# Kernel tuning notes

Measured on AMD Instinct MI355X. Metric: run time of the kernel, lower is better.

The kernel has to match this reference:

```python
import jax, jax.numpy as jnp
import numpy as np

B, S, D, H = 2, 2048, 2048, 16
DK = D // H  # 128
ROPE_BASE = 10000.0


def _rope_tables(seq_len, d_k, dtype=jnp.float32):
    # cos/sin of shape [1, S, 1, d_k], duplicated halves as in the torch module
    inv_freq = 1.0 / (ROPE_BASE ** (jnp.arange(0, d_k, 2, dtype=jnp.float32) / d_k))
    pos = jnp.arange(seq_len, dtype=jnp.float32)
    freqs = jnp.outer(pos, inv_freq)               # [S, d_k/2]
    cos = jnp.concatenate([jnp.cos(freqs), jnp.cos(freqs)], axis=-1)  # [S, d_k]
    sin = jnp.concatenate([jnp.sin(freqs), jnp.sin(freqs)], axis=-1)
    return cos[None, :, None, :].astype(dtype), sin[None, :, None, :].astype(dtype)


def _rotate_half(x):
    d = x.shape[-1]
    x1, x2 = x[..., : d // 2], x[..., d // 2 :]
    return jnp.concatenate([-x2, x1], axis=-1)


def setup_inputs() -> dict:
    key = jax.random.key(0)
    ks = jax.random.split(key, 5)
    scale = 1.0 / np.sqrt(D)
    x = jax.random.normal(ks[0], (B, S, D), dtype=jnp.float32)
    Wq = jax.random.normal(ks[1], (D, D), dtype=jnp.float32) * scale
    Wk = jax.random.normal(ks[2], (D, D), dtype=jnp.float32) * scale
    Wv = jax.random.normal(ks[3], (D, D), dtype=jnp.float32) * scale
    Wo = jax.random.normal(ks[4], (D, D), dtype=jnp.float32) * scale
    bq = jnp.zeros((D,), jnp.float32)
    bk = jnp.zeros((D,), jnp.float32)
    bv = jnp.zeros((D,), jnp.float32)
    bo = jnp.zeros((D,), jnp.float32)
    mask = jnp.tril(jnp.ones((S, S), dtype=bool))[None, None]  # causal [1,1,S,S]
    return {"x": x, "mask": mask, "Wq": Wq, "bq": bq, "Wk": Wk, "bk": bk,
            "Wv": Wv, "bv": bv, "Wo": Wo, "bo": bo}


def reference(x, mask, Wq, bq, Wk, bk, Wv, bv, Wo, bo):
    b, s, d = x.shape
    # torch nn.Linear: y = x @ W.T + b
    Q = (x @ Wq.T + bq).reshape(b, s, H, DK)
    K = (x @ Wk.T + bk).reshape(b, s, H, DK)
    V = (x @ Wv.T + bv).reshape(b, s, H, DK)
    cos, sin = _rope_tables(s, DK, x.dtype)
    Q = Q * cos + _rotate_half(Q) * sin
    K = K * cos + _rotate_half(K) * sin
    # [b, h, s, dk]
    Q = Q.transpose(0, 2, 1, 3)
    K = K.transpose(0, 2, 1, 3)
    V = V.transpose(0, 2, 1, 3)
    scores = jnp.einsum("bhqd,bhkd->bhqk", Q, K) / jnp.sqrt(jnp.asarray(DK, x.dtype))
    scores = jnp.where(mask, scores, jnp.asarray(-jnp.inf, x.dtype))
    attn = jax.nn.softmax(scores, axis=-1)
    out = jnp.einsum("bhqk,bhkd->bhqd", attn, V)
    out = out.transpose(0, 2, 1, 3).reshape(b, s, d)
    return out @ Wo.T + bo
```

## Files before the change

kernel.cpp:

```cpp
#include <hip/hip_runtime.h>

typedef unsigned short u16;
typedef __attribute__((ext_vector_type(8))) short short8;
typedef __attribute__((ext_vector_type(4))) float f32x4;
typedef __attribute__((ext_vector_type(4))) unsigned short u16x4;

__device__ __forceinline__ float bf2f(u16 h){
  unsigned u = ((unsigned)h) << 16; float f; __builtin_memcpy(&f, &u, 4); return f;
}
__device__ __forceinline__ u16 f2bf(float f){
  unsigned u; __builtin_memcpy(&u, &f, 4);
  unsigned r = u + 0x7fffu + ((u >> 16) & 1u);
  return (u16)(r >> 16);
}

__device__ __forceinline__ void glds16(const u16* g, u16* l){
  __builtin_amdgcn_global_load_lds(
      (const __attribute__((address_space(1))) unsigned int*)(const void*)g,
      (__attribute__((address_space(3))) unsigned int*)(void*)l, 16, 0, 0);
}

__global__ __launch_bounds__(256) void cvt_all(const float* __restrict__ x,
    const float* __restrict__ w0, const float* __restrict__ w1,
    const float* __restrict__ w2, const float* __restrict__ w3,
    u16* __restrict__ xb, u16* __restrict__ wb){
  int blk = blockIdx.x;
  const float* src; u16* dst; int i;
  if (blk < 8192){
    src = x; dst = xb; i = blk * 256 + threadIdx.x;
  } else {
    int b2 = blk - 8192;
    int which = b2 >> 12;
    src = (which == 0) ? w0 : (which == 1) ? w1 : (which == 2) ? w2 : w3;
    dst = wb + (size_t)which * 4194304;
    i = (b2 & 4095) * 256 + threadIdx.x;
  }
  float4 f = ((const float4*)src)[i];
  u16x4 o; o.x = f2bf(f.x); o.y = f2bf(f.y); o.z = f2bf(f.z); o.w = f2bf(f.w);
  ((u16x4*)dst)[i] = o;
}

__global__ __launch_bounds__(256, 4) void gemm_bt(
    const u16* __restrict__ A, const u16* __restrict__ Bm, int mode,
    u16* __restrict__ qws, u16* __restrict__ kws, u16* __restrict__ vws,
    const float* __restrict__ bq, const float* __restrict__ bk, const float* __restrict__ bv,
    float* __restrict__ outf, const float* __restrict__ bo)
{
  const int K = 2048;
  __shared__ __attribute__((aligned(16))) u16 As[128 * 64];
  __shared__ __attribute__((aligned(16))) u16 Bs[128 * 64];

  int tid = threadIdx.x, wave = tid >> 6, lane = tid & 63;
  int quad = lane >> 4, l15 = lane & 15;
  int wm = wave >> 1, wn = wave & 1;

  size_t rowA0 = (size_t)blockIdx.y * 128;
  size_t rowB0 = (size_t)blockIdx.x * 128;

  int lrow0 = tid >> 3;
  int c0 = (tid & 7) ^ (lrow0 & 7);
  const u16* gA = A  + (rowA0 + lrow0) * K + c0 * 8;
  const u16* gB = Bm + (rowB0 + lrow0) * K + c0 * 8;
  u16* lA = As + (size_t)(wave * 64) * 8;
  u16* lB = Bs + (size_t)(wave * 64) * 8;

  f32x4 acc[4][4];
  #pragma unroll
  for (int i = 0; i < 4; i++)
    #pragma unroll
    for (int j = 0; j < 4; j++) acc[i][j] = f32x4{0.f, 0.f, 0.f, 0.f};

  int aoff[4], boff[4];
  #pragma unroll
  for (int t = 0; t < 4; t++){
    int ra = wm * 64 + t * 16 + l15;
    aoff[t] = ra * 64 + ((quad ^ (ra & 7)) * 8);
    int rb = wn * 32 + (t >> 1) * 64 + (t & 1) * 16 + l15;
    boff[t] = rb * 64 + ((quad ^ (rb & 7)) * 8);
  }

  for (int k0 = 0; k0 < K; k0 += 64){
    __syncthreads();
    #pragma unroll
    for (int ri = 0; ri < 4; ri++){
      glds16(gA + ri * 65536, lA + ri * 2048);
      glds16(gB + ri * 65536, lB + ri * 2048);
    }
    gA += 64; gB += 64;
    __syncthreads();
    #pragma unroll
    for (int kk = 0; kk < 2; kk++){
      const int kx = kk * 32;
      short8 af[4], bfr[4];
      #pragma unroll
      for (int t = 0; t < 4; t++){
        af[t]  = *(const short8*)(As + (aoff[t] ^ kx));
        bfr[t] = *(const short8*)(Bs + (boff[t] ^ kx));
      }
      #pragma unroll
      for (int i = 0; i < 4; i++)
        #pragma unroll
        for (int j = 0; j < 4; j++)
          acc[i][j] = __builtin_amdgcn_mfma_f32_16x16x32_bf16(af[i], bfr[j], acc[i][j], 0, 0, 0);
    }
  }

  if (mode == 0){
    int col0 = (int)rowB0;
    int mat = col0 >> 11;
    int cm  = col0 & 2047;
    const float* bias = (mat == 0) ? bq : (mat == 1) ? bk : bv;
    int b  = (int)(rowA0 >> 11);
    int s0 = (int)(rowA0 & 2047);
    int h  = cm >> 7;
    size_t base = ((size_t)(b * 16 + h)) * 2048 * 128;
    if (mat == 2){
      #pragma unroll
      for (int j = 0; j < 4; j++){
        int d = wn * 32 + (j >> 1) * 64 + (j & 1) * 16 + l15;
        float bv_ = bias[cm + d];
        #pragma unroll
        for (int i = 0; i < 4; i++){
          int srow = s0 + wm * 64 + i * 16 + quad * 4;
          u16x4 pk;
          #pragma unroll
          for (int r = 0; r < 4; r++) pk[r] = f2bf(acc[i][j][r] + bv_);
          *(u16x4*)(vws + base + (size_t)d * 2048 + srow) = pk;
        }
      }
    } else {
      u16* dst = (mat == 0) ? qws : kws;
      #pragma unroll
      for (int jp = 0; jp < 2; jp++){
        int dlow = wn * 32 + jp * 16 + l15;
        float bias_lo = bias[cm + dlow];
        float bias_hi = bias[cm + dlow + 64];
        float invf = __expf(-0.14391156831212788f * (float)dlow);
        #pragma unroll
        for (int i = 0; i < 4; i++){
          int srow0 = s0 + wm * 64 + i * 16 + quad * 4;
          #pragma unroll
          for (int r = 0; r < 4; r++){
            float a  = acc[i][jp][r]     + bias_lo;
            float b2 = acc[i][jp + 2][r] + bias_hi;
            float th = (float)(srow0 + r) * invf;
            float sn, cs; __sincosf(th, &sn, &cs);
            size_t ro = base + (size_t)(srow0 + r) * 128;
            dst[ro + dlow]      = f2bf(a * cs - b2 * sn);
            dst[ro + dlow + 64] = f2bf(b2 * cs + a * sn);
          }
        }
      }
    }
  } else {
    int col0 = (int)rowB0;
    #pragma unroll
    for (int j = 0; j < 4; j++){
      int c = col0 + wn * 32 + (j >> 1) * 64 + (j & 1) * 16 + l15;
      float bo_ = bo[c];
      #pragma unroll
      for (int i = 0; i < 4; i++){
        int rg = (int)rowA0 + wm * 64 + i * 16 + quad * 4;
        #pragma unroll
        for (int r = 0; r < 4; r++)
          outf[(size_t)(rg + r) * 2048 + c] = acc[i][j][r] + bo_;
      }
    }
  }
}

__global__ __launch_bounds__(256, 2) void flash(
    const u16* __restrict__ Q, const u16* __restrict__ Km, const u16* __restrict__ VT,
    u16* __restrict__ O)
{
  __shared__ __attribute__((aligned(16))) u16 Ks[2][64 * 128];
  __shared__ __attribute__((aligned(16))) u16 Vs[2][128 * 64];
  __shared__ __attribute__((aligned(16))) u16 PL[4 * 16 * 64];
  const float scale = 0.08838834764831845f;

  int id = (int)(blockIdx.x + (blockIdx.y << 4));
  int xcd = id & 7;
  int kk_ = id >> 3;
  int bh = xcd + ((kk_ >> 4) << 3);
  int pr = kk_ & 15;
  int tid = threadIdx.x, wave = tid >> 6, lane = tid & 63;
  int quad = lane >> 4, l15 = lane & 15;

  const u16* Qb = Q  + (size_t)bh * 2048 * 128;
  const u16* Kb = Km + (size_t)bh * 2048 * 128;
  const u16* Vb = VT + (size_t)bh * 2048 * 128;
  u16* PW = PL + wave * (16 * 64);

  int krow0 = tid >> 4;
  const u16* gK0 = Kb + (size_t)krow0 * 128 + ((tid & 15) ^ (krow0 & 15)) * 8;
  int vd0 = tid >> 3;
  const u16* gV0 = Vb + (size_t)vd0 * 2048 + ((tid & 7) ^ (vd0 & 7)) * 8;
  int lOff0 = wave * 512;

  for (int phase = 0; phase < 2; phase++){
    int qtile = phase ? (31 - pr) : pr;
    int qw = qtile * 64 + wave * 16;

    short8 qf[4];
    {
      const u16* qr = Qb + (size_t)(qw + l15) * 128 + quad * 8;
      #pragma unroll
      for (int c = 0; c < 4; c++) qf[c] = *(const short8*)(qr + c * 32);
    }

    float mr[4], lr[4]; f32x4 o[8];
    #pragma unroll
    for (int r = 0; r < 4; r++){ mr[r] = -1e30f; lr[r] = 0.f; }
    #pragma unroll
    for (int blk = 0; blk < 8; blk++) o[blk] = f32x4{0.f, 0.f, 0.f, 0.f};

    int niter = qtile + 1;

    __syncthreads();
    #pragma unroll
    for (int r = 0; r < 4; r++){
      glds16(gK0 + r * 2048,  Ks[0] + lOff0 + r * 2048);
      glds16(gV0 + r * 65536, Vs[0] + lOff0 + r * 2048);
    }

    for (int it = 0; it < niter; it++){
      int k0 = it * 64;
      int buf = it & 1;
      __syncthreads();
      if (it + 1 < niter){
        int nb = buf ^ 1;
        #pragma unroll
        for (int r = 0; r < 4; r++){
          glds16(gK0 + (size_t)(k0 + 64) * 128 + r * 2048, Ks[nb] + lOff0 + r * 2048);
          glds16(gV0 + (k0 + 64) + r * 65536,              Vs[nb] + lOff0 + r * 2048);
        }
      }
      const u16* KsB = Ks[buf];
      const u16* VsB = Vs[buf];

      int rel = qw + 15 - k0;
      int smax = rel >> 4; if (smax > 3) smax = 3;
      float sreg[4][4];
      #pragma unroll
      for (int t = 0; t < 4; t++){
        if (t <= smax){
          short8 kf[4];
          #pragma unroll
          for (int c = 0; c < 4; c++)
            kf[c] = *(const short8*)(KsB + (t * 16 + l15) * 128 + (((c * 4 + quad) ^ l15) * 8));
          f32x4 a = f32x4{0.f, 0.f, 0.f, 0.f};
          #pragma unroll
          for (int c = 0; c < 4; c++)
            a = __builtin_amdgcn_mfma_f32_16x16x32_bf16(qf[c], kf[c], a, 0, 0, 0);
          int kvcol = k0 + t * 16 + l15;
          #pragma unroll
          for (int r = 0; r < 4; r++){
            float v = a[r] * scale;
            int row = qw + quad * 4 + r;
            if (kvcol > row) v = -1e30f;
            sreg[t][r] = v;
          }
        }
      }
      float px[4];
      #pragma unroll
      for (int r = 0; r < 4; r++){
        float x = sreg[0][r];
        #pragma unroll
        for (int t = 1; t < 4; t++) if (t <= smax) x = fmaxf(x, sreg[t][r]);
        x = fmaxf(x, __shfl_xor(x, 1));
        x = fmaxf(x, __shfl_xor(x, 2));
        x = fmaxf(x, __shfl_xor(x, 4));
        x = fmaxf(x, __shfl_xor(x, 8));
        px[r] = x;
      }
      float g01 = fmaxf(px[0] - mr[0], px[1] - mr[1]);
      float g23 = fmaxf(px[2] - mr[2], px[3] - mr[3]);
      int noresc = __all(fmaxf(g01, g23) <= 8.0f);
      float alpha[4];
      if (!noresc){
        #pragma unroll
        for (int r = 0; r < 4; r++){
          float mn = fmaxf(mr[r], px[r]);
          alpha[r] = __expf(mr[r] - mn);
          mr[r] = mn;
        }
      }
      float lsum[4];
      #pragma unroll
      for (int r = 0; r < 4; r++) lsum[r] = 0.f;
      #pragma unroll
      for (int t = 0; t < 4; t++){
        if (t <= smax){
          int chi = t * 2 + (l15 >> 3);
          #pragma unroll
          for (int r = 0; r < 4; r++){
            float p = __expf(sreg[t][r] - mr[r]);
            lsum[r] += p;
            int row = quad * 4 + r;
            PW[row * 64 + ((chi ^ (row & 7)) << 3) + (l15 & 7)] = f2bf(p);
          }
        }
      }
      if (!(smax & 1)){
        int chi = (smax + 1) * 2 + (l15 >> 3);
        #pragma unroll
        for (int r = 0; r < 4; r++){
          int row = quad * 4 + r;
          PW[row * 64 + ((chi ^ (row & 7)) << 3) + (l15 & 7)] = 0;
        }
      }
      #pragma unroll
      for (int r = 0; r < 4; r++){
        float sv = lsum[r];
        sv += __shfl_xor(sv, 1); sv += __shfl_xor(sv, 2);
        sv += __shfl_xor(sv, 4); sv += __shfl_xor(sv, 8);
        lr[r] = noresc ? (lr[r] + sv) : (lr[r] * alpha[r] + sv);
      }
      if (!noresc){
        #pragma unroll
        for (int blk = 0; blk < 8; blk++){
          o[blk][0] *= alpha[0]; o[blk][1] *= alpha[1];
          o[blk][2] *= alpha[2]; o[blk][3] *= alpha[3];
        }
      }
      __builtin_amdgcn_s_waitcnt(0xC07F);
      int nch = (smax >> 1) + 1;
      #pragma unroll
      for (int c2 = 0; c2 < 2; c2++){
        if (c2 < nch){
          short8 pf = *(const short8*)(PW + l15 * 64 + (((c2 * 4 + quad) ^ (l15 & 7)) << 3));
          #pragma unroll
          for (int blk = 0; blk < 8; blk++){
            int d = blk * 16 + l15;
            short8 vf = *(const short8*)(VsB + d * 64 + (((c2 * 4 + quad) ^ (l15 & 7)) * 8));
            o[blk] = __builtin_amdgcn_mfma_f32_16x16x32_bf16(pf, vf, o[blk], 0, 0, 0);
          }
        }
      }
    }

    int b = bh >> 4, h = bh & 15;
    float inv[4];
    #pragma unroll
    for (int r = 0; r < 4; r++) inv[r] = 1.0f / lr[r];
    #pragma unroll
    for (int blk = 0; blk < 8; blk++){
      int d = h * 128 + blk * 16 + l15;
      #pragma unroll
      for (int r = 0; r < 4; r++){
        int srow = qw + quad * 4 + r;
        O[((size_t)(b * 2048 + srow)) * 2048 + d] = f2bf(o[blk][r] * inv[r]);
      }
    }
  }
}

extern "C" void kernel_launch(void* const* d_in, const int* in_sizes, int n_in,
                              void* d_out, int out_size, void* d_ws, size_t ws_size,
                              hipStream_t stream)
{
  const float* x  = (const float*)d_in[0];
  const float* Wq = (const float*)d_in[2];
  const float* bq = (const float*)d_in[3];
  const float* Wk = (const float*)d_in[4];
  const float* bk = (const float*)d_in[5];
  const float* Wv = (const float*)d_in[6];
  const float* bv = (const float*)d_in[7];
  const float* Wo = (const float*)d_in[8];
  const float* bo = (const float*)d_in[9];
  float* out = (float*)d_out;

  char* ws = (char*)d_ws;
  u16* xb   = (u16*)(ws);
  u16* wcat = (u16*)(ws + 16777216);
  u16* wob  = (u16*)(ws + 41943040);
  u16* qws  = (u16*)(ws + 50331648);
  u16* kws  = (u16*)(ws + 67108864);
  u16* vws  = (u16*)(ws + 83886080);
  u16* attn = (u16*)(ws + 100663296);

  cvt_all<<<24576, 256, 0, stream>>>(x, Wq, Wk, Wv, Wo, xb, wcat);

  gemm_bt<<<dim3(48, 32), 256, 0, stream>>>(xb, wcat, 0, qws, kws, vws,
                                            bq, bk, bv, nullptr, nullptr);
  flash<<<dim3(16, 32), 256, 0, stream>>>(qws, kws, vws, attn);
  gemm_bt<<<dim3(16, 32), 256, 0, stream>>>(attn, wob, 1, nullptr, nullptr, nullptr,
                                            nullptr, nullptr, nullptr, out, bo);
}
```

Before: 404.6 us.

## Split flash KV loop across two wave groups and read V from global

The flash kernel now launches 512 threads so two groups of four waves each process alternating 64-key tiles of the same query tile. Afterwards the groups merge their softmax max/sum and partial outputs through shared memory. V tiles are no longer staged in LDS and are loaded straight from global memory into MFMA operands. This halves the serial KV iteration count per block, at the cost of a multi-barrier merge step, higher register pressure under launch_bounds(512,4), and possibly slower uncoalesced V reads.

```diff
diff --git a/kernel.cpp b/kernel.cpp
--- a/kernel.cpp
+++ b/kernel.cpp
@@ -169,13 +169,12 @@
   }
 }
 
-__global__ __launch_bounds__(256, 2) void flash(
+__global__ __launch_bounds__(512, 4) void flash(
     const u16* __restrict__ Q, const u16* __restrict__ Km, const u16* __restrict__ VT,
     u16* __restrict__ O)
 {
-  __shared__ __attribute__((aligned(16))) u16 Ks[2][64 * 128];
-  __shared__ __attribute__((aligned(16))) u16 Vs[2][128 * 64];
-  __shared__ __attribute__((aligned(16))) u16 PL[4 * 16 * 64];
+  __shared__ __attribute__((aligned(16))) u16 Ks[2][2][64 * 128];
+  __shared__ __attribute__((aligned(16))) u16 PL[8 * 16 * 64];
   const float scale = 0.08838834764831845f;
 
   int id = (int)(blockIdx.x + (blockIdx.y << 4));
@@ -183,23 +182,24 @@
   int kk_ = id >> 3;
   int bh = xcd + ((kk_ >> 4) << 3);
   int pr = kk_ & 15;
-  int tid = threadIdx.x, wave = tid >> 6, lane = tid & 63;
+  int tid = threadIdx.x;
+  int w = tid >> 6, lane = tid & 63;
+  int g = w >> 2, ws = w & 3;
   int quad = lane >> 4, l15 = lane & 15;
 
   const u16* Qb = Q  + (size_t)bh * 2048 * 128;
   const u16* Kb = Km + (size_t)bh * 2048 * 128;
   const u16* Vb = VT + (size_t)bh * 2048 * 128;
-  u16* PW = PL + wave * (16 * 64);
-
-  int krow0 = tid >> 4;
-  const u16* gK0 = Kb + (size_t)krow0 * 128 + ((tid & 15) ^ (krow0 & 15)) * 8;
-  int vd0 = tid >> 3;
-  const u16* gV0 = Vb + (size_t)vd0 * 2048 + ((tid & 7) ^ (vd0 & 7)) * 8;
-  int lOff0 = wave * 512;
+  u16* PW = PL + w * 1024;
+  float* fPL = (float*)PL;
+
+  int tl = ws * 64 + lane;
+  int krow0 = tl >> 4;
+  const u16* gK0 = Kb + (size_t)krow0 * 128 + ((tl & 15) ^ (krow0 & 15)) * 8;
 
   for (int phase = 0; phase < 2; phase++){
     int qtile = phase ? (31 - pr) : pr;
-    int qw = qtile * 64 + wave * 16;
+    int qw = qtile * 64 + ws * 16;
 
     short8 qf[4];
     {
@@ -215,142 +215,201 @@
     for (int blk = 0; blk < 8; blk++) o[blk] = f32x4{0.f, 0.f, 0.f, 0.f};
 
     int niter = qtile + 1;
-
-    __syncthreads();
-    #pragma unroll
-    for (int r = 0; r < 4; r++){
-      glds16(gK0 + r * 2048,  Ks[0] + lOff0 + r * 2048);
-      glds16(gV0 + r * 65536, Vs[0] + lOff0 + r * 2048);
-    }
-
-    for (int it = 0; it < niter; it++){
-      int k0 = it * 64;
-      int buf = it & 1;
+    int ca = (niter + 1) >> 1;
+    int cb = niter >> 1;
+    int myn = g ? cb : ca;
+
+    __syncthreads();
+    if (g < niter){
+      const u16* src = gK0 + (size_t)g * 8192;
+      u16* dst = Ks[g][0] + ws * 512;
+      #pragma unroll
+      for (int r = 0; r < 4; r++) glds16(src + r * 2048, dst + r * 2048);
+    }
+
+    for (int i = 0; i < ca; i++){
       __syncthreads();
-      if (it + 1 < niter){
-        int nb = buf ^ 1;
+      int tn = 2 * (i + 1) + g;
+      if (tn < niter){
+        const u16* src = gK0 + (size_t)tn * 8192;
+        u16* dst = Ks[g][(i + 1) & 1] + ws * 512;
+        #pragma unroll
+        for (int r = 0; r < 4; r++) glds16(src + r * 2048, dst + r * 2048);
+      }
+      if (i < myn){
+        int k0 = (2 * i + g) * 64;
+        const u16* KsB = Ks[g][i & 1];
+
+        int rel = qw + 15 - k0;
+        int smax = rel >> 4; if (smax > 3) smax = 3;
+        float sreg[4][4];
+        #pragma unroll
+        for (int t = 0; t < 4; t++){
+          if (t <= smax){
+            short8 kf[4];
+            #pragma unroll
+            for (int c = 0; c < 4; c++)
+              kf[c] = *(const short8*)(KsB + (t * 16 + l15) * 128 + (((c * 4 + quad) ^ l15) * 8));
+            f32x4 a = f32x4{0.f, 0.f, 0.f, 0.f};
+            #pragma unroll
+            for (int c = 0; c < 4; c++)
+              a = __builtin_amdgcn_mfma_f32_16x16x32_bf16(qf[c], kf[c], a, 0, 0, 0);
+            int kvcol = k0 + t * 16 + l15;
+            #pragma unroll
+            for (int r = 0; r < 4; r++){
+              float v = a[r] * scale;
+              int row = qw + quad * 4 + r;
+              if (kvcol > row) v = -1e30f;
+              sreg[t][r] = v;
+            }
+          }
+        }
+        float px[4];
         #pragma unroll
         for (int r = 0; r < 4; r++){
-          glds16(gK0 + (size_t)(k0 + 64) * 128 + r * 2048, Ks[nb] + lOff0 + r * 2048);
-          glds16(gV0 + (k0 + 64) + r * 65536,              Vs[nb] + lOff0 + r * 2048);
-        }
-      }
-      const u16* KsB = Ks[buf];
-      const u16* VsB = Vs[buf];
-
-      int rel = qw + 15 - k0;
-      int smax = rel >> 4; if (smax > 3) smax = 3;
-      float sreg[4][4];
-      #pragma unroll
-      for (int t = 0; t < 4; t++){
-        if (t <= smax){
-          short8 kf[4];
-          #pragma unroll
-          for (int c = 0; c < 4; c++)
-            kf[c] = *(const short8*)(KsB + (t * 16 + l15) * 128 + (((c * 4 + quad) ^ l15) * 8));
-          f32x4 a = f32x4{0.f, 0.f, 0.f, 0.f};
-          #pragma unroll
-          for (int c = 0; c < 4; c++)
-            a = __builtin_amdgcn_mfma_f32_16x16x32_bf16(qf[c], kf[c], a, 0, 0, 0);
-          int kvcol = k0 + t * 16 + l15;
+          float x = sreg[0][r];
+          #pragma unroll
+          for (int t = 1; t < 4; t++) if (t <= smax) x = fmaxf(x, sreg[t][r]);
+          x = fmaxf(x, __shfl_xor(x, 1));
+          x = fmaxf(x, __shfl_xor(x, 2));
+          x = fmaxf(x, __shfl_xor(x, 4));
+          x = fmaxf(x, __shfl_xor(x, 8));
+          px[r] = x;
+        }
+        float g01 = fmaxf(px[0] - mr[0], px[1] - mr[1]);
+        float g23 = fmaxf(px[2] - mr[2], px[3] - mr[3]);
+        int noresc = __all(fmaxf(g01, g23) <= 8.0f);
+        float alpha[4];
+        if (!noresc){
           #pragma unroll
           for (int r = 0; r < 4; r++){
-            float v = a[r] * scale;
-            int row = qw + quad * 4 + r;
-            if (kvcol > row) v = -1e30f;
-            sreg[t][r] = v;
-          }
-        }
-      }
-      float px[4];
+            float mn = fmaxf(mr[r], px[r]);
+            alpha[r] = __expf(mr[r] - mn);
+            mr[r] = mn;
+          }
+        }
+        float lsum[4];
+        #pragma unroll
+        for (int r = 0; r < 4; r++) lsum[r] = 0.f;
+        #pragma unroll
+        for (int t = 0; t < 4; t++){
+          if (t <= smax){
+            int chi = t * 2 + (l15 >> 3);
+            #pragma unroll
+            for (int r = 0; r < 4; r++){
+              float p = __expf(sreg[t][r] - mr[r]);
+              lsum[r] += p;
+              int row = quad * 4 + r;
+              PW[row * 64 + ((chi ^ (row & 7)) << 3) + (l15 & 7)] = f2bf(p);
+            }
+          }
+        }
+        if (!(smax & 1)){
+          int chi = (smax + 1) * 2 + (l15 >> 3);
+          #pragma unroll
+          for (int r = 0; r < 4; r++){
+            int row = quad * 4 + r;
+            PW[row * 64 + ((chi ^ (row & 7)) << 3) + (l15 & 7)] = 0;
+          }
+        }
+        #pragma unroll
+        for (int r = 0; r < 4; r++){
+          float sv = lsum[r];
+          sv += __shfl_xor(sv, 1); sv += __shfl_xor(sv, 2);
+          sv += __shfl_xor(sv, 4); sv += __shfl_xor(sv, 8);
+          lr[r] = noresc ? (lr[r] + sv) : (lr[r] * alpha[r] + sv);
+        }
+        if (!noresc){
+          #pragma unroll
+          for (int blk = 0; blk < 8; blk++){
+            o[blk][0] *= alpha[0]; o[blk][1] *= alpha[1];
+            o[blk][2] *= alpha[2]; o[blk][3] *= alpha[3];
+          }
+        }
+        __builtin_amdgcn_s_waitcnt(0xC07F);
+        int nch = (smax >> 1) + 1;
+        #pragma unroll
+        for (int c2 = 0; c2 < 2; c2++){
+          if (c2 < nch){
+            short8 pf = *(const short8*)(PW + l15 * 64 + (((c2 * 4 + quad) ^ (l15 & 7)) << 3));
+            const u16* vbase = Vb + k0 + c2 * 32 + quad * 8;
+            #pragma unroll
+            for (int blk = 0; blk < 8; blk++){
+              short8 vf = *(const short8*)(vbase + (size_t)(blk * 16 + l15) * 2048);
+              o[blk] = __builtin_amdgcn_mfma_f32_16x16x32_bf16(pf, vf, o[blk], 0, 0, 0);
+            }
+          }
+        }
+      }
+    }
+
+    __syncthreads();
+    if (l15 == 0){
       #pragma unroll
       for (int r = 0; r < 4; r++){
-        float x = sreg[0][r];
-        #pragma unroll
-        for (int t = 1; t < 4; t++) if (t <= smax) x = fmaxf(x, sreg[t][r]);
-        x = fmaxf(x, __shfl_xor(x, 1));
-        x = fmaxf(x, __shfl_xor(x, 2));
-        x = fmaxf(x, __shfl_xor(x, 4));
-        x = fmaxf(x, __shfl_xor(x, 8));
-        px[r] = x;
-      }
-      float g01 = fmaxf(px[0] - mr[0], px[1] - mr[1]);
-      float g23 = fmaxf(px[2] - mr[2], px[3] - mr[3]);
-      int noresc = __all(fmaxf(g01, g23) <= 8.0f);
-      float alpha[4];
-      if (!noresc){
+        int row = quad * 4 + r;
+        fPL[(w * 16 + row) * 2 + 0] = mr[r];
+        fPL[(w * 16 + row) * 2 + 1] = lr[r];
+      }
+    }
+    __syncthreads();
+    float sOwn[4], lstar[4];
+    {
+      int pw = w ^ 4;
+      #pragma unroll
+      for (int r = 0; r < 4; r++){
+        int row = quad * 4 + r;
+        float mo = fPL[(pw * 16 + row) * 2 + 0];
+        float lo = fPL[(pw * 16 + row) * 2 + 1];
+        float ms = fmaxf(mr[r], mo);
+        sOwn[r] = __expf(mr[r] - ms);
+        lstar[r] = lr[r] * sOwn[r] + lo * __expf(mo - ms);
+      }
+    }
+    __syncthreads();
+    float* ob = fPL + ws * 1024;
+    if (g == 1){
+      #pragma unroll
+      for (int blk = 0; blk < 4; blk++)
+        #pragma unroll
+        for (int r = 0; r < 4; r++)
+          ob[(blk * 16 + l15) * 16 + quad * 4 + r] = o[blk][r] * sOwn[r];
+    }
+    __syncthreads();
+    if (g == 0){
+      #pragma unroll
+      for (int blk = 0; blk < 4; blk++)
+        #pragma unroll
+        for (int r = 0; r < 4; r++)
+          o[blk][r] = o[blk][r] * sOwn[r] + ob[(blk * 16 + l15) * 16 + quad * 4 + r];
+    }
+    __syncthreads();
+    if (g == 1){
+      #pragma unroll
+      for (int blk = 4; blk < 8; blk++)
+        #pragma unroll
+        for (int r = 0; r < 4; r++)
+          ob[((blk - 4) * 16 + l15) * 16 + quad * 4 + r] = o[blk][r] * sOwn[r];
+    }
+    __syncthreads();
+    if (g == 0){
+      #pragma unroll
+      for (int blk = 4; blk < 8; blk++)
+        #pragma unroll
+        for (int r = 0; r < 4; r++)
+          o[blk][r] = o[blk][r] * sOwn[r] + ob[((blk - 4) * 16 + l15) * 16 + quad * 4 + r];
+      int b = bh >> 4, h = bh & 15;
+      float inv[4];
+      #pragma unroll
+      for (int r = 0; r < 4; r++) inv[r] = 1.0f / lstar[r];
+      #pragma unroll
+      for (int blk = 0; blk < 8; blk++){
+        int d = h * 128 + blk * 16 + l15;
         #pragma unroll
         for (int r = 0; r < 4; r++){
-          float mn = fmaxf(mr[r], px[r]);
-          alpha[r] = __expf(mr[r] - mn);
-          mr[r] = mn;
-        }
-      }
-      float lsum[4];
-      #pragma unroll
-      for (int r = 0; r < 4; r++) lsum[r] = 0.f;
-      #pragma unroll
-      for (int t = 0; t < 4; t++){
-        if (t <= smax){
-          int chi = t * 2 + (l15 >> 3);
-          #pragma unroll
-          for (int r = 0; r < 4; r++){
-            float p = __expf(sreg[t][r] - mr[r]);
-            lsum[r] += p;
-            int row = quad * 4 + r;
-            PW[row * 64 + ((chi ^ (row & 7)) << 3) + (l15 & 7)] = f2bf(p);
-          }
-        }
-      }
-      if (!(smax & 1)){
-        int chi = (smax + 1) * 2 + (l15 >> 3);
-        #pragma unroll
-        for (int r = 0; r < 4; r++){
-          int row = quad * 4 + r;
-          PW[row * 64 + ((chi ^ (row & 7)) << 3) + (l15 & 7)] = 0;
-        }
-      }
-      #pragma unroll
-      for (int r = 0; r < 4; r++){
-        float sv = lsum[r];
-        sv += __shfl_xor(sv, 1); sv += __shfl_xor(sv, 2);
-        sv += __shfl_xor(sv, 4); sv += __shfl_xor(sv, 8);
-        lr[r] = noresc ? (lr[r] + sv) : (lr[r] * alpha[r] + sv);
-      }
-      if (!noresc){
-        #pragma unroll
-        for (int blk = 0; blk < 8; blk++){
-          o[blk][0] *= alpha[0]; o[blk][1] *= alpha[1];
-          o[blk][2] *= alpha[2]; o[blk][3] *= alpha[3];
-        }
-      }
-      __builtin_amdgcn_s_waitcnt(0xC07F);
-      int nch = (smax >> 1) + 1;
-      #pragma unroll
-      for (int c2 = 0; c2 < 2; c2++){
-        if (c2 < nch){
-          short8 pf = *(const short8*)(PW + l15 * 64 + (((c2 * 4 + quad) ^ (l15 & 7)) << 3));
-          #pragma unroll
-          for (int blk = 0; blk < 8; blk++){
-            int d = blk * 16 + l15;
-            short8 vf = *(const short8*)(VsB + d * 64 + (((c2 * 4 + quad) ^ (l15 & 7)) * 8));
-            o[blk] = __builtin_amdgcn_mfma_f32_16x16x32_bf16(pf, vf, o[blk], 0, 0, 0);
-          }
-        }
-      }
-    }
-
-    int b = bh >> 4, h = bh & 15;
-    float inv[4];
-    #pragma unroll
-    for (int r = 0; r < 4; r++) inv[r] = 1.0f / lr[r];
-    #pragma unroll
-    for (int blk = 0; blk < 8; blk++){
-      int d = h * 128 + blk * 16 + l15;
-      #pragma unroll
-      for (int r = 0; r < 4; r++){
-        int srow = qw + quad * 4 + r;
-        O[((size_t)(b * 2048 + srow)) * 2048 + d] = f2bf(o[blk][r] * inv[r]);
+          int srow = qw + quad * 4 + r;
+          O[((size_t)(b * 2048 + srow)) * 2048 + d] = f2bf(o[blk][r] * inv[r]);
+        }
       }
     }
   }
@@ -384,7 +443,7 @@
 
   gemm_bt<<<dim3(48, 32), 256, 0, stream>>>(xb, wcat, 0, qws, kws, vws,
                                             bq, bk, bv, nullptr, nullptr);
-  flash<<<dim3(16, 32), 256, 0, stream>>>(qws, kws, vws, attn);
+  flash<<<dim3(16, 32), 512, 0, stream>>>(qws, kws, vws, attn);
   gemm_bt<<<dim3(16, 32), 256, 0, stream>>>(attn, wob, 1, nullptr, nullptr, nullptr,
                                             nullptr, nullptr, nullptr, out, bo);
 }
```

Measured after the change: 534.9 us. 1.32x slower.
